# Optimization experiments

Hardware: AMD Instinct MI355X
Metric: run time of the kernel (lower is better)

## Reference

```python
import jax, jax.numpy as jnp
import numpy as np

D_MODEL = 1024
N_HEAD = 16
D_K = D_MODEL // N_HEAD


def setup_inputs() -> dict:
    key = jax.random.key(0)
    ks = jax.random.split(key, 11)
    B, S = 2, 2048
    std = 1.0 / np.sqrt(D_MODEL)
    inp = {
        "Q": jax.random.normal(ks[0], (B, S, D_MODEL), jnp.float32),
        "K": jax.random.normal(ks[1], (B, S, D_MODEL), jnp.float32),
        "V": jax.random.normal(ks[2], (B, S, D_MODEL), jnp.float32),
        "Wq": jax.random.normal(ks[3], (D_MODEL, D_MODEL), jnp.float32) * std,
        "bq": jnp.zeros((D_MODEL,), jnp.float32),
        "Wk": jax.random.normal(ks[4], (D_MODEL, D_MODEL), jnp.float32) * std,
        "bk": jnp.zeros((D_MODEL,), jnp.float32),
        "Wv": jax.random.normal(ks[5], (D_MODEL, D_MODEL), jnp.float32) * std,
        "bv": jnp.zeros((D_MODEL,), jnp.float32),
        "Wo": jax.random.normal(ks[6], (D_MODEL, D_MODEL), jnp.float32) * std,
        "bo": jnp.zeros((D_MODEL,), jnp.float32),
    }
    return inp


def _split_heads(x):
    # [B, S, D] -> [B, H, S, d_k]
    B, S, _ = x.shape
    return x.reshape(B, S, N_HEAD, D_K).transpose(0, 2, 1, 3)


def reference(Q, K, V, Wq, bq, Wk, bk, Wv, bv, Wo, bo):
    q = _split_heads(Q @ Wq.T + bq)   # [B,H,S,dk]
    k = _split_heads(K @ Wk.T + bk)
    v = _split_heads(V @ Wv.T + bv)
    scale = 1.0 / jnp.sqrt(jnp.float32(D_K))
    scores = jnp.einsum("bhqd,bhkd->bhqk", q, k) * scale
    attn = jax.nn.softmax(scores, axis=-1)
    ctx = jnp.einsum("bhqk,bhkd->bhqd", attn, v)  # [B,H,S,dk]
    B, H, S, dk = ctx.shape
    ctx = ctx.transpose(0, 2, 1, 3).reshape(B, S, H * dk)
    return ctx @ Wo.T + bo
```

## Files before the change

kernel.cpp:

```cpp
#include <hip/hip_runtime.h>
#include <hip/hip_bf16.h>
#include <cstdint>
#include <cstddef>
#include <cmath>

typedef __attribute__((ext_vector_type(8))) short short8;
typedef __attribute__((ext_vector_type(4))) short short4_t;
typedef __attribute__((ext_vector_type(4))) float f32x4;
typedef __attribute__((ext_vector_type(16))) float f32x16;

constexpr int B_ = 2, S_ = 2048, H_ = 16, DK_ = 64, DM_ = 1024;

__device__ inline unsigned short f2bf(float x) {
  union { float f; unsigned u; } c; c.f = x;
  unsigned r = c.u + 0x7FFF + ((c.u >> 16) & 1);
  return (unsigned short)(r >> 16);
}

__device__ inline float ex2(float x) {
#if __has_builtin(__builtin_amdgcn_exp2f)
  return __builtin_amdgcn_exp2f(x);
#else
  return exp2f(x);
#endif
}

__device__ inline unsigned pkbf(float lo, float hi) {
  unsigned u;
  asm("v_cvt_pk_bf16_f32 %0, %1, %2" : "=v"(u) : "v"(lo), "v"(hi));
  return u;
}

__device__ inline void plswap(unsigned& a, unsigned& b) {
#if __has_builtin(__builtin_amdgcn_permlane32_swap)
  auto r = __builtin_amdgcn_permlane32_swap(a, b, false, false);
  a = (unsigned)r[0];
  b = (unsigned)r[1];
#else
  unsigned sa = __shfl_xor(a, 32), sb = __shfl_xor(b, 32);
  unsigned lid = __builtin_amdgcn_mbcnt_hi(~0u, __builtin_amdgcn_mbcnt_lo(~0u, 0));
  bool hi = lid >= 32;
  unsigned na = hi ? sb : a;
  unsigned nb = hi ? b : sa;
  a = na; b = nb;
#endif
}

__device__ inline float red_half_sum(float x) {
  unsigned a = __float_as_uint(x), b = a;
  plswap(a, b);
  return __uint_as_float(a) + __uint_as_float(b);
}

__device__ inline f32x4 mfma16(short8 a, short8 b, f32x4 c) {
  return __builtin_amdgcn_mfma_f32_16x16x32_bf16(a, b, c, 0, 0, 0);
}
__device__ inline f32x16 mfma32(short8 a, short8 b, f32x16 c) {
  return __builtin_amdgcn_mfma_f32_32x32x16_bf16(a, b, c, 0, 0, 0);
}

__device__ inline void glds16(const unsigned short* g, unsigned short* l) {
  __builtin_amdgcn_global_load_lds(
      (const __attribute__((address_space(1))) unsigned int*)g,
      (__attribute__((address_space(3))) unsigned int*)l, 16, 0, 0);
}

__global__ __launch_bounds__(256) void cvt_all(
    const float* __restrict__ Q, const float* __restrict__ K,
    const float* __restrict__ V, const float* __restrict__ Wq,
    const float* __restrict__ Wk, const float* __restrict__ Wv,
    const float* __restrict__ Wo, unsigned short* __restrict__ Qb,
    unsigned short* __restrict__ Kb, unsigned short* __restrict__ Vb,
    unsigned short* __restrict__ Wqb, unsigned short* __restrict__ Wkb,
    unsigned short* __restrict__ Wvb, unsigned short* __restrict__ Wob) {
  int bid = blockIdx.x;
  const float* in; unsigned short* out; int off;
  if (bid < 4096)       { in = Q;  out = Qb;  off = bid; }
  else if (bid < 8192)  { in = K;  out = Kb;  off = bid - 4096; }
  else if (bid < 12288) { in = V;  out = Vb;  off = bid - 8192; }
  else if (bid < 13312) { in = Wq; out = Wqb; off = bid - 12288; }
  else if (bid < 14336) { in = Wk; out = Wkb; off = bid - 13312; }
  else if (bid < 15360) { in = Wv; out = Wvb; off = bid - 14336; }
  else                  { in = Wo; out = Wob; off = bid - 15360; }
  int i = off * 256 + threadIdx.x;
  float4 f = ((const float4*)in)[i];
  uint2 o;
  o.x = pkbf(f.x, f.y);
  o.y = pkbf(f.z, f.w);
  ((uint2*)out)[i] = o;
}

__device__ inline void store_out(float* p, float v) { *p = v; }
__device__ inline void store_out(unsigned short* p, float v) { *p = f2bf(v); }

template <typename OUT_T>
__device__ inline void gemm128_body(const unsigned short* __restrict__ A,
                                    const unsigned short* __restrict__ Bw,
                                    const float* __restrict__ bias,
                                    OUT_T* __restrict__ C, float cscale,
                                    int bm, int bn) {
  constexpr int Kd = 1024, Nd = 1024;
  __shared__ unsigned short As[128][64];
  __shared__ unsigned short Bs[128][64];

  const int tid = threadIdx.x;
  const int lane = tid & 63, wave = tid >> 6;
  const int li = lane & 15, lg = lane >> 4;
  const int wm = wave >> 1, wn = wave & 1;

  const f32x4 zero4 = {0.f, 0.f, 0.f, 0.f};
  f32x4 acc[4][4];
#pragma unroll
  for (int i = 0; i < 4; i++)
#pragma unroll
    for (int j = 0; j < 4; j++) acc[i][j] = zero4;

  const int srow = tid >> 3;
  const int scol = (tid & 7) * 8;
  const unsigned short* Ag = A + (size_t)(bm * 128 + srow) * Kd + scol;
  const unsigned short* Bg = Bw + (size_t)(bn * 128 + srow) * Kd + scol;

  for (int kt = 0; kt < Kd; kt += 64) {
#pragma unroll
    for (int i = 0; i < 4; i++) {
      glds16(Ag + (size_t)(i * 32) * Kd + kt, &As[i * 32 + srow][scol]);
      glds16(Bg + (size_t)(i * 32) * Kd + kt, &Bs[i * 32 + srow][scol]);
    }
    __syncthreads();

    short8 af[4][2], bf[4][2];
#pragma unroll
    for (int kb = 0; kb < 2; kb++)
#pragma unroll
      for (int i = 0; i < 4; i++) {
        af[i][kb] = *(const short8*)&As[wm * 64 + i * 16 + li][kb * 32 + lg * 8];
        bf[i][kb] = *(const short8*)&Bs[wn * 64 + i * 16 + li][kb * 32 + lg * 8];
      }
#pragma unroll
    for (int kb = 0; kb < 2; kb++)
#pragma unroll
      for (int i = 0; i < 4; i++)
#pragma unroll
        for (int j = 0; j < 4; j++)
          acc[i][j] = mfma16(af[i][kb], bf[j][kb], acc[i][j]);
    __syncthreads();
  }

#pragma unroll
  for (int j = 0; j < 4; j++) {
    int col = bn * 128 + wn * 64 + j * 16 + li;
    float bv = bias[col];
#pragma unroll
    for (int i = 0; i < 4; i++) {
      int row0 = bm * 128 + wm * 64 + i * 16 + lg * 4;
#pragma unroll
      for (int r = 0; r < 4; r++)
        store_out(&C[(size_t)(row0 + r) * Nd + col], (acc[i][j][r] + bv) * cscale);
    }
  }
}

__global__ __launch_bounds__(256) void gemm_qkv(
    const unsigned short* __restrict__ Aq, const unsigned short* __restrict__ Ak,
    const unsigned short* __restrict__ Av, const unsigned short* __restrict__ Bq,
    const unsigned short* __restrict__ Bk, const unsigned short* __restrict__ Bv,
    const float* __restrict__ bq, const float* __restrict__ bk,
    const float* __restrict__ bv, unsigned short* __restrict__ Cq,
    unsigned short* __restrict__ Ck, unsigned short* __restrict__ Cv,
    float qscale) {
  const int z = blockIdx.z;
  const unsigned short* A = z == 0 ? Aq : z == 1 ? Ak : Av;
  const unsigned short* Bw = z == 0 ? Bq : z == 1 ? Bk : Bv;
  const float* bi = z == 0 ? bq : z == 1 ? bk : bv;
  unsigned short* C = z == 0 ? Cq : z == 1 ? Ck : Cv;
  gemm128_body(A, Bw, bi, C, z == 0 ? qscale : 1.0f, blockIdx.x, blockIdx.y);
}

__global__ __launch_bounds__(256) void gemm_out(
    const unsigned short* __restrict__ A, const unsigned short* __restrict__ Bw,
    const float* __restrict__ bias, float* __restrict__ C) {
  gemm128_body(A, Bw, bias, C, 1.0f, blockIdx.x, blockIdx.y);
}

struct V4 { short8 v[4]; };

__device__ __forceinline__ void attn_tile_step(
    int kt, int buf, int NT,
    const unsigned short* kg, const unsigned short* vg,
    unsigned short* KsAll, unsigned short* VtAll,
    int srow, int sc, int scs, int key2, int dq,
    const short8* qf, int l31, int h,
    V4& vc, V4& vn, f32x16* po, float& l_lane) {
  unsigned short* KsB = KsAll + buf * (128 * 64);
  unsigned short* VtB = VtAll + buf * (64 * 128);
  unsigned short* KsO = KsAll + (buf ^ 1) * (128 * 64);

  asm volatile("s_waitcnt vmcnt(0)" ::: "memory");
  __builtin_amdgcn_sched_barrier(0);

#pragma unroll
  for (int j = 0; j < 16; j++) {
    const int half = j >> 3, jj = j & 7;
    unsigned w = (unsigned)(unsigned short)vc.v[half][jj] |
                 ((unsigned)(unsigned short)vc.v[2 + half][jj] << 16);
    const int slot = (key2 >> 3) ^ j;
    *(unsigned*)&VtB[(dq * 16 + j) * 128 + slot * 8 + (key2 & 7)] = w;
  }

  if (kt + 1 < NT) {
    const unsigned short* vp =
        vg + (size_t)((kt + 1) * 128 + key2) * DM_ + dq * 16;
    vn.v[0] = *(const short8*)(vp);
    vn.v[1] = *(const short8*)(vp + 8);
    vn.v[2] = *(const short8*)(vp + DM_);
    vn.v[3] = *(const short8*)(vp + DM_ + 8);
  }

  asm volatile("s_waitcnt lgkmcnt(0)" ::: "memory");
  __builtin_amdgcn_sched_barrier(0);
  __builtin_amdgcn_s_barrier();
  __builtin_amdgcn_sched_barrier(0);

  if (kt + 1 < NT) {
    const unsigned short* kgt = kg + (size_t)((kt + 1) * 128) * DM_;
#pragma unroll
    for (int i = 0; i < 4; i++)
      glds16(kgt + (size_t)(i * 32 + srow) * DM_ + scs,
             &KsO[(i * 32 + srow) * 64 + sc * 8]);
  }
  __builtin_amdgcn_sched_barrier(0);

  f32x16 sacc[4];
#pragma unroll
  for (int kb = 0; kb < 4; kb++)
#pragma unroll
    for (int r = 0; r < 16; r++) sacc[kb][r] = 0.f;

  __builtin_amdgcn_s_setprio(1);
#pragma unroll
  for (int tq = 0; tq < 4; tq++) {
    const int sl = ((((tq << 1) | h) ^ (l31 & 7))) * 8;
#pragma unroll
    for (int kb = 0; kb < 4; kb++) {
      short8 kf = *(const short8*)&KsB[(kb * 32 + l31) * 64 + sl];
      sacc[kb] = mfma32(kf, qf[tq], sacc[kb]);
    }
  }
  __builtin_amdgcn_s_setprio(0);

  float s0 = 0.f, s1 = 0.f, s2 = 0.f, s3 = 0.f;
#pragma unroll
  for (int kb = 0; kb < 4; kb++) {
#pragma unroll
    for (int r = 0; r < 16; r += 4) {
      float p0 = ex2(sacc[kb][r]);
      float p1 = ex2(sacc[kb][r + 1]);
      float p2 = ex2(sacc[kb][r + 2]);
      float p3 = ex2(sacc[kb][r + 3]);
      sacc[kb][r] = p0; sacc[kb][r + 1] = p1;
      sacc[kb][r + 2] = p2; sacc[kb][r + 3] = p3;
      s0 += p0; s1 += p1; s2 += p2; s3 += p3;
    }
    unsigned u[4][2];
#pragma unroll
    for (int qd = 0; qd < 4; qd++) {
      u[qd][0] = pkbf(sacc[kb][4 * qd], sacc[kb][4 * qd + 1]);
      u[qd][1] = pkbf(sacc[kb][4 * qd + 2], sacc[kb][4 * qd + 3]);
    }
    __builtin_amdgcn_s_setprio(1);
#pragma unroll
    for (int tt = 0; tt < 2; tt++) {
      const int tp = 2 * kb + tt;
      unsigned x0 = u[2 * tt][0], x1 = u[2 * tt][1];
      unsigned y0 = u[2 * tt + 1][0], y1 = u[2 * tt + 1][1];
      plswap(x0, y0);
      plswap(x1, y1);
      union { unsigned w[4]; short8 v8; } fr;
      fr.w[0] = x0;
      fr.w[1] = x1;
      fr.w[2] = y0;
      fr.w[3] = y1;
      const int slbase = (tp << 1) | h;
#pragma unroll
      for (int db = 0; db < 2; db++) {
        const int row = db * 32 + l31;
        short8 vf = *(const short8*)
            &VtB[row * 128 + (slbase ^ (l31 & 15)) * 8];
        po[db] = mfma32(vf, fr.v8, po[db]);
      }
    }
    __builtin_amdgcn_s_setprio(0);
  }
  l_lane += (s0 + s1) + (s2 + s3);
}

__global__ __launch_bounds__(256, 2) void attn_fwd(
    const unsigned short* __restrict__ q, const unsigned short* __restrict__ k,
    const unsigned short* __restrict__ v, unsigned short* __restrict__ ctx) {
  __shared__ unsigned short Ks[2][128][64];
  __shared__ unsigned short Vt[2][64][128];

  const int tid = threadIdx.x;
  const int lane = tid & 63, wave = tid >> 6;
  const int l31 = lane & 31, h = lane >> 5;
  const int n = blockIdx.x;
  const int xcd = n & 7, m = n >> 3;
  const int bh = xcd * 4 + (m & 3);
  const int qt = m >> 2;
  const int b = bh >> 4, hd = bh & 15;

  const int qrow = qt * 128 + wave * 32 + l31;
  const unsigned short* qg = q + (size_t)(b * S_ + qrow) * DM_ + hd * DK_;
  short8 qf[4];
#pragma unroll
  for (int t = 0; t < 4; t++) qf[t] = *(const short8*)(qg + t * 16 + h * 8);

  f32x16 po[2];
#pragma unroll
  for (int db = 0; db < 2; db++)
#pragma unroll
    for (int r = 0; r < 16; r++) po[db][r] = 0.f;
  float l_lane = 0.f;

  const int srow = tid >> 3, sc = tid & 7;
  const int scs = (sc ^ (srow & 7)) * 8;
  const unsigned short* kg = k + (size_t)(b * S_) * DM_ + hd * DK_;

  const int key2 = (tid & 63) * 2, dq = tid >> 6;
  const unsigned short* vg = v + (size_t)(b * S_) * DM_ + hd * DK_;

  const int NT = S_ / 128;

#pragma unroll
  for (int i = 0; i < 4; i++)
    glds16(kg + (size_t)(i * 32 + srow) * DM_ + scs,
           &Ks[0][i * 32 + srow][sc * 8]);
  V4 va, vb;
  {
    const unsigned short* vp = vg + (size_t)key2 * DM_ + dq * 16;
    va.v[0] = *(const short8*)(vp);
    va.v[1] = *(const short8*)(vp + 8);
    va.v[2] = *(const short8*)(vp + DM_);
    va.v[3] = *(const short8*)(vp + DM_ + 8);
  }

  unsigned short* KsAll = &Ks[0][0][0];
  unsigned short* VtAll = &Vt[0][0][0];
  for (int it = 0; it < NT; it += 2) {
    attn_tile_step(it, 0, NT, kg, vg, KsAll, VtAll, srow, sc, scs, key2, dq,
                   qf, l31, h, va, vb, po, l_lane);
    attn_tile_step(it + 1, 1, NT, kg, vg, KsAll, VtAll, srow, sc, scs, key2,
                   dq, qf, l31, h, vb, va, po, l_lane);
  }

  float l_i = red_half_sum(l_lane);
  float rl = 1.0f / l_i;
  unsigned short* cg = ctx + (size_t)(b * S_ + qrow) * DM_ + hd * DK_;
#pragma unroll
  for (int db = 0; db < 2; db++)
#pragma unroll
    for (int rq = 0; rq < 4; rq++) {
      uint2 w2;
      w2.x = pkbf(po[db][4 * rq] * rl, po[db][4 * rq + 1] * rl);
      w2.y = pkbf(po[db][4 * rq + 2] * rl, po[db][4 * rq + 3] * rl);
      *(uint2*)(cg + db * 32 + 8 * rq + 4 * h) = w2;
    }
}

extern "C" void kernel_launch(void* const* d_in, const int* in_sizes, int n_in,
                              void* d_out, int out_size, void* d_ws, size_t ws_size,
                              hipStream_t stream) {
  const float* Q  = (const float*)d_in[0];
  const float* Kx = (const float*)d_in[1];
  const float* V  = (const float*)d_in[2];
  const float* Wq = (const float*)d_in[3];
  const float* bq = (const float*)d_in[4];
  const float* Wk = (const float*)d_in[5];
  const float* bk = (const float*)d_in[6];
  const float* Wv = (const float*)d_in[7];
  const float* bv = (const float*)d_in[8];
  const float* Wo = (const float*)d_in[9];
  const float* bo = (const float*)d_in[10];
  float* out = (float*)d_out;

  char* ws = (char*)d_ws;
  const size_t MB = 1ull << 20;
  unsigned short* Qb  = (unsigned short*)(ws + 0 * MB);
  unsigned short* Kb  = (unsigned short*)(ws + 8 * MB);
  unsigned short* Vb  = (unsigned short*)(ws + 16 * MB);
  unsigned short* Wqb = (unsigned short*)(ws + 24 * MB);
  unsigned short* Wkb = (unsigned short*)(ws + 26 * MB);
  unsigned short* Wvb = (unsigned short*)(ws + 28 * MB);
  unsigned short* Wob = (unsigned short*)(ws + 30 * MB);
  unsigned short* qp  = (unsigned short*)(ws + 32 * MB);
  unsigned short* kp  = (unsigned short*)(ws + 40 * MB);
  unsigned short* vp  = (unsigned short*)(ws + 48 * MB);
  unsigned short* cx  = (unsigned short*)(ws + 56 * MB);

  cvt_all<<<16384, 256, 0, stream>>>(Q, Kx, V, Wq, Wk, Wv, Wo,
                                     Qb, Kb, Vb, Wqb, Wkb, Wvb, Wob);

  gemm_qkv<<<dim3(32, 8, 3), 256, 0, stream>>>(
      Qb, Kb, Vb, Wqb, Wkb, Wvb, bq, bk, bv, qp, kp, vp, 0.18033688f);

  attn_fwd<<<512, 256, 0, stream>>>(qp, kp, vp, cx);

  gemm_out<<<dim3(32, 8), 256, 0, stream>>>(cx, Wob, bo, out);
}
```

Before: 135.1 us.

## Triple-buffer GEMM K-loop and shrink N-tile to 64 for more blocks

Replaces the single-buffered 128x128 GEMM body with a 128x64 tile and a three-stage LDS ring. Global-to-LDS loads run two steps ahead, gated by partial vmcnt waits and one barrier per step instead of two. The grid doubles in N so the 1024-wide projections launch more blocks and fill the CUs better, and launch bounds request two blocks per CU. The cost is more LDS per block (about 72KB), less operand reuse per tile, and more redundant A-tile loads.

```diff
diff --git a/kernel.cpp b/kernel.cpp
--- a/kernel.cpp
+++ b/kernel.cpp
@@ -94,14 +94,14 @@
 __device__ inline void store_out(unsigned short* p, float v) { *p = f2bf(v); }
 
 template <typename OUT_T>
-__device__ inline void gemm128_body(const unsigned short* __restrict__ A,
+__device__ inline void gemm_k3_body(const unsigned short* __restrict__ A,
                                     const unsigned short* __restrict__ Bw,
                                     const float* __restrict__ bias,
                                     OUT_T* __restrict__ C, float cscale,
                                     int bm, int bn) {
-  constexpr int Kd = 1024, Nd = 1024;
-  __shared__ unsigned short As[128][64];
-  __shared__ unsigned short Bs[128][64];
+  constexpr int Kd = 1024, Nd = 1024, NSTEP = Kd / 64;
+  __shared__ unsigned short As[3][128][64];
+  __shared__ unsigned short Bs[3][64][64];
 
   const int tid = threadIdx.x;
   const int lane = tid & 63, wave = tid >> 6;
@@ -109,46 +109,76 @@
   const int wm = wave >> 1, wn = wave & 1;
 
   const f32x4 zero4 = {0.f, 0.f, 0.f, 0.f};
-  f32x4 acc[4][4];
+  f32x4 acc[4][2];
 #pragma unroll
   for (int i = 0; i < 4; i++)
 #pragma unroll
-    for (int j = 0; j < 4; j++) acc[i][j] = zero4;
-
-  const int srow = tid >> 3;
-  const int scol = (tid & 7) * 8;
-  const unsigned short* Ag = A + (size_t)(bm * 128 + srow) * Kd + scol;
-  const unsigned short* Bg = Bw + (size_t)(bn * 128 + srow) * Kd + scol;
-
-  for (int kt = 0; kt < Kd; kt += 64) {
-#pragma unroll
-    for (int i = 0; i < 4; i++) {
-      glds16(Ag + (size_t)(i * 32) * Kd + kt, &As[i * 32 + srow][scol]);
-      glds16(Bg + (size_t)(i * 32) * Kd + kt, &Bs[i * 32 + srow][scol]);
-    }
-    __syncthreads();
-
-    short8 af[4][2], bf[4][2];
+    for (int j = 0; j < 2; j++) acc[i][j] = zero4;
+
+  const int stg_row = tid >> 3;
+  const int stg_col = (tid & 7) * 8;
+  const unsigned short* Ag = A + (size_t)(bm * 128 + stg_row) * Kd + stg_col;
+  const unsigned short* Bg = Bw + (size_t)(bn * 64 + stg_row) * Kd + stg_col;
+
+  auto stage = [&](int s, int kt) {
+    const int kof = kt * 64;
+#pragma unroll
+    for (int i = 0; i < 4; i++)
+      glds16(Ag + (size_t)(i * 32) * Kd + kof,
+             &As[s][i * 32 + stg_row][stg_col]);
+#pragma unroll
+    for (int i = 0; i < 2; i++)
+      glds16(Bg + (size_t)(i * 32) * Kd + kof,
+             &Bs[s][i * 32 + stg_row][stg_col]);
+  };
+
+  stage(0, 0);
+  stage(1, 1);
+
+  int buf = 0;
+  for (int kt = 0; kt < NSTEP; kt++) {
+    if (kt < NSTEP - 1)
+      asm volatile("s_waitcnt vmcnt(6)" ::: "memory");
+    else
+      asm volatile("s_waitcnt vmcnt(0)" ::: "memory");
+    __builtin_amdgcn_sched_barrier(0);
+    __builtin_amdgcn_s_barrier();
+    __builtin_amdgcn_sched_barrier(0);
+
+    if (kt + 2 < NSTEP) {
+      int nb = buf + 2;
+      if (nb >= 3) nb -= 3;
+      stage(nb, kt + 2);
+    }
+    __builtin_amdgcn_sched_barrier(0);
+
+    short8 af[4][2], bf[2][2];
+#pragma unroll
+    for (int kb = 0; kb < 2; kb++) {
+#pragma unroll
+      for (int i = 0; i < 4; i++)
+        af[i][kb] =
+            *(const short8*)&As[buf][wm * 64 + i * 16 + li][kb * 32 + lg * 8];
+#pragma unroll
+      for (int j = 0; j < 2; j++)
+        bf[j][kb] =
+            *(const short8*)&Bs[buf][wn * 32 + j * 16 + li][kb * 32 + lg * 8];
+    }
 #pragma unroll
     for (int kb = 0; kb < 2; kb++)
 #pragma unroll
-      for (int i = 0; i < 4; i++) {
-        af[i][kb] = *(const short8*)&As[wm * 64 + i * 16 + li][kb * 32 + lg * 8];
-        bf[i][kb] = *(const short8*)&Bs[wn * 64 + i * 16 + li][kb * 32 + lg * 8];
-      }
-#pragma unroll
-    for (int kb = 0; kb < 2; kb++)
-#pragma unroll
       for (int i = 0; i < 4; i++)
 #pragma unroll
-        for (int j = 0; j < 4; j++)
+        for (int j = 0; j < 2; j++)
           acc[i][j] = mfma16(af[i][kb], bf[j][kb], acc[i][j]);
-    __syncthreads();
-  }
-
-#pragma unroll
-  for (int j = 0; j < 4; j++) {
-    int col = bn * 128 + wn * 64 + j * 16 + li;
+
+    buf++;
+    if (buf == 3) buf = 0;
+  }
+
+#pragma unroll
+  for (int j = 0; j < 2; j++) {
+    int col = bn * 64 + wn * 32 + j * 16 + li;
     float bv = bias[col];
 #pragma unroll
     for (int i = 0; i < 4; i++) {
@@ -160,7 +190,7 @@
   }
 }
 
-__global__ __launch_bounds__(256) void gemm_qkv(
+__global__ __launch_bounds__(256, 2) void gemm_qkv(
     const unsigned short* __restrict__ Aq, const unsigned short* __restrict__ Ak,
     const unsigned short* __restrict__ Av, const unsigned short* __restrict__ Bq,
     const unsigned short* __restrict__ Bk, const unsigned short* __restrict__ Bv,
@@ -173,13 +203,13 @@
   const unsigned short* Bw = z == 0 ? Bq : z == 1 ? Bk : Bv;
   const float* bi = z == 0 ? bq : z == 1 ? bk : bv;
   unsigned short* C = z == 0 ? Cq : z == 1 ? Ck : Cv;
-  gemm128_body(A, Bw, bi, C, z == 0 ? qscale : 1.0f, blockIdx.x, blockIdx.y);
-}
-
-__global__ __launch_bounds__(256) void gemm_out(
+  gemm_k3_body(A, Bw, bi, C, z == 0 ? qscale : 1.0f, blockIdx.x, blockIdx.y);
+}
+
+__global__ __launch_bounds__(256, 2) void gemm_out(
     const unsigned short* __restrict__ A, const unsigned short* __restrict__ Bw,
     const float* __restrict__ bias, float* __restrict__ C) {
-  gemm128_body(A, Bw, bias, C, 1.0f, blockIdx.x, blockIdx.y);
+  gemm_k3_body(A, Bw, bias, C, 1.0f, blockIdx.x, blockIdx.y);
 }
 
 struct V4 { short8 v[4]; };
@@ -400,10 +430,10 @@
   cvt_all<<<16384, 256, 0, stream>>>(Q, Kx, V, Wq, Wk, Wv, Wo,
                                      Qb, Kb, Vb, Wqb, Wkb, Wvb, Wob);
 
-  gemm_qkv<<<dim3(32, 8, 3), 256, 0, stream>>>(
+  gemm_qkv<<<dim3(32, 16, 3), 256, 0, stream>>>(
       Qb, Kb, Vb, Wqb, Wkb, Wvb, bq, bk, bv, qp, kp, vp, 0.18033688f);
 
   attn_fwd<<<512, 256, 0, stream>>>(qp, kp, vp, cx);
 
-  gemm_out<<<dim3(32, 8), 256, 0, stream>>>(cx, Wob, bo, out);
-}
+  gemm_out<<<dim3(32, 16), 256, 0, stream>>>(cx, Wob, bo, out);
+}
```

After: 134.6 us. No clear change (-0.4%).
